# Optimization experiments

Hardware: AMD Instinct MI355X
Metric: run time of the kernel (lower is better)

The kernel has to match this reference:

```python
import jax, jax.numpy as jnp
import numpy as np

N_NODES = 50000


def _sage_conv(x, edge_index, W_l, W_r, b):
    """PyG SAGEConv (aggr='mean', root_weight=True):
    out[i] = mean_{j: (j->i) in E} x[j] @ W_l + x[i] @ W_r + b
    """
    src, dst = edge_index[0], edge_index[1]
    msgs = x[src]                                   # [E, d] gather
    agg = jax.ops.segment_sum(msgs, dst, num_segments=N_NODES)  # [N, d]
    deg = jax.ops.segment_sum(jnp.ones_like(dst, dtype=x.dtype), dst,
                              num_segments=N_NODES)
    agg = agg / jnp.maximum(deg, 1.0)[:, None]      # mean aggregation
    return agg @ W_l + x @ W_r + b


def setup_inputs() -> dict:
    key = jax.random.key(0)
    ks = jax.random.split(key, 8)
    d_in, d_hid, d_out = 128, 128, 64
    n_edges = 640000
    x = jax.random.normal(ks[0], (N_NODES, d_in), dtype=jnp.float32)
    edge_index = jax.random.randint(ks[1], (2, n_edges), 0, N_NODES, dtype=jnp.int32)
    s1 = 1.0 / np.sqrt(d_in)
    s2 = 1.0 / np.sqrt(d_hid)
    return {
        "x": x,
        "edge_index": edge_index,
        "W1_l": jax.random.uniform(ks[2], (d_in, d_hid), jnp.float32, -s1, s1),
        "W1_r": jax.random.uniform(ks[3], (d_in, d_hid), jnp.float32, -s1, s1),
        "b1": jnp.zeros((d_hid,), jnp.float32),
        "W2_l": jax.random.uniform(ks[4], (d_hid, d_out), jnp.float32, -s2, s2),
        "W2_r": jax.random.uniform(ks[5], (d_hid, d_out), jnp.float32, -s2, s2),
        "b2": jnp.zeros((d_out,), jnp.float32),
    }


def reference(x, edge_index, W1_l, W1_r, b1, W2_l, W2_r, b2):
    h = _sage_conv(x, edge_index, W1_l, W1_r, b1)
    h = jax.nn.relu(h)
    # Dropout(0.3) is identity in eval mode.
    return _sage_conv(h, edge_index, W2_l, W2_r, b2)
```

## Files before the change

kernel.cpp:

```cpp
#include <hip/hip_runtime.h>
#include <hip/hip_fp16.h>


typedef _Float16 half8 __attribute__((ext_vector_type(8)));
typedef float floatx4 __attribute__((ext_vector_type(4)));

#define NB 256
#define PA 320
#define HB 320

__global__ __launch_bounds__(256) void prep_hist_kernel(const float* __restrict__ x,
                                                        const float* __restrict__ W1l, const float* __restrict__ W1r,
                                                        const float* __restrict__ W2l, const float* __restrict__ W2r,
                                                        _Float16* __restrict__ Ah,
                                                        _Float16* __restrict__ Bp1, _Float16* __restrict__ Bp2,
                                                        const int* __restrict__ dst, int* __restrict__ ghist,
                                                        int N, int E, int nper) {
    __shared__ int lh[NB];
    int nconv = (N * 16 + 255) / 256;
    int b = blockIdx.x;
    int tid = threadIdx.x;
    if (b < nconv) {
        int i = b * 256 + tid;
        if (i < N * 16) {
            int row = i >> 4, c = i & 15;
            const float4* xp = (const float4*)x;
            float4 v0 = xp[(size_t)row * 32 + c * 2];
            float4 v1 = xp[(size_t)row * 32 + c * 2 + 1];
            __half2 h0 = __floats2half2_rn(v0.x, v0.y);
            __half2 h1 = __floats2half2_rn(v0.z, v0.w);
            __half2 h2 = __floats2half2_rn(v1.x, v1.y);
            __half2 h3 = __floats2half2_rn(v1.z, v1.w);
            uint4 o;
            o.x = *(const uint*)&h0; o.y = *(const uint*)&h1;
            o.z = *(const uint*)&h2; o.w = *(const uint*)&h3;
            *(uint4*)(Ah + (size_t)row * 256 + 128 + c * 8) = o;
        }
    } else if (b < nconv + 128) {
        int t = (b - nconv) * 256 + tid;
        int j = t & 7, lane = (t >> 3) & 63, nrep = (t >> 9) & 7, kt = t >> 12;
        int k = kt * 32 + ((lane >> 4) * 8) + j;
        int col = nrep * 16 + (lane & 15);
        float v = (k < 128) ? W1l[k * 128 + col] : W1r[(k - 128) * 128 + col];
        Bp1[t] = (_Float16)v;
    } else if (b < nconv + 192) {
        int t = (b - nconv - 128) * 256 + tid;
        int j = t & 7, lane = (t >> 3) & 63, nrep = (t >> 9) & 7, kt = t >> 12;
        int k = kt * 32 + ((lane >> 4) * 8) + j;
        int col = nrep * 16 + (lane & 15);
        float v = (col < 64) ? W2l[k * 64 + col] : W2r[k * 64 + (col - 64)];
        Bp2[t] = (_Float16)v;
    } else {
        int hb = b - nconv - 192;
        lh[tid] = 0;
        __syncthreads();
        int chunk = (E + HB - 1) / HB;
        int e0 = hb * chunk, e1 = min(e0 + chunk, E);
        for (int e = e0 + tid; e < e1; e += 256) atomicAdd(&lh[dst[e] / nper], 1);
        __syncthreads();
        int c = lh[tid];
        if (c) atomicAdd(&ghist[tid], c);
    }
}

__global__ __launch_bounds__(256) void partA_kernel(const int* __restrict__ src, const int* __restrict__ dst,
                                                    const int* __restrict__ ghist, int* __restrict__ bcur,
                                                    unsigned int* __restrict__ bek,
                                                    int E, int nper) {
    __shared__ int cnt[NB], base[NB], cur[NB];
    __shared__ int ws[4], wo[4];
    int tid = threadIdx.x;
    int v = ghist[tid];
    int lane = tid & 63, wid = tid >> 6;
    int s = v;
#pragma unroll
    for (int off = 1; off < 64; off <<= 1) { int t = __shfl_up(s, off); if (lane >= off) s += t; }
    if (lane == 63) ws[wid] = s;
    cnt[tid] = 0; cur[tid] = 0;
    __syncthreads();
    if (tid == 0) { int a = 0; for (int w = 0; w < 4; ++w) { wo[w] = a; a += ws[w]; } }
    __syncthreads();
    int excl = s + wo[wid] - v;
    int chunk = (E + PA - 1) / PA;
    int e0 = blockIdx.x * chunk;
    int e1 = min(e0 + chunk, E);
    for (int e = e0 + tid; e < e1; e += 256) {
        int d = dst[e];
        atomicAdd(&cnt[d / nper], 1);
    }
    __syncthreads();
    int c = cnt[tid];
    base[tid] = excl + ((c > 0) ? atomicAdd(&bcur[tid], c) : 0);
    __syncthreads();
    for (int e = e0 + tid; e < e1; e += 256) {
        int d = dst[e];
        int b = d / nper;
        int pos = base[b] + atomicAdd(&cur[b], 1);
        bek[pos] = ((unsigned int)src[e] << 8) | (unsigned int)(d - b * nper);
    }
}

__global__ __launch_bounds__(256) void partB2_kernel(const unsigned int* __restrict__ bek,
                                                     const int* __restrict__ ghist,
                                                     int* __restrict__ rp, float* __restrict__ inv,
                                                     int* __restrict__ csr, int N, int nper) {
    __shared__ int gh[NB], exg[NB];
    __shared__ int lcnt[256], excl[256], cur[256];
    __shared__ int ws[4], wo[4];
    int k = blockIdx.x;
    int lo = k * nper;
    int hi = min(lo + nper, N);
    int cntN = hi - lo;
    if (cntN <= 0) return;
    int tid = threadIdx.x;
    int lane = tid & 63, wid = tid >> 6;
    int v = ghist[tid];
    gh[tid] = v;
    int s = v;
#pragma unroll
    for (int off = 1; off < 64; off <<= 1) { int t = __shfl_up(s, off); if (lane >= off) s += t; }
    if (lane == 63) ws[wid] = s;
    lcnt[tid] = 0; cur[tid] = 0;
    __syncthreads();
    if (tid == 0) { int a = 0; for (int w = 0; w < 4; ++w) { wo[w] = a; a += ws[w]; } }
    __syncthreads();
    exg[tid] = s + wo[wid] - v;
    __syncthreads();
    int ebeg = exg[k], eend = ebeg + gh[k];
    for (int j = ebeg + tid; j < eend; j += 256)
        atomicAdd(&lcnt[bek[j] & 0xffu], 1);
    __syncthreads();
    int v2 = lcnt[tid];
    int s2 = v2;
#pragma unroll
    for (int off = 1; off < 64; off <<= 1) { int t = __shfl_up(s2, off); if (lane >= off) s2 += t; }
    if (lane == 63) ws[wid] = s2;
    __syncthreads();
    if (tid == 0) { int a = 0; for (int w = 0; w < 4; ++w) { wo[w] = a; a += ws[w]; } }
    __syncthreads();
    excl[tid] = s2 + wo[wid] - v2;
    __syncthreads();
    if (tid <= cntN) {
        int node = lo + tid;
        if (node <= N) rp[node] = ebeg + excl[tid];
        if (tid < cntN) inv[node] = 1.0f / fmaxf((float)lcnt[tid], 1.0f);
    }
    for (int j = ebeg + tid; j < eend; j += 256) {
        unsigned int u = bek[j];
        int loc = (int)(u & 0xffu);
        int pos = ebeg + excl[loc] + atomicAdd(&cur[loc], 1);
        csr[pos] = (int)(u >> 8);
    }
}

__global__ __launch_bounds__(256) void agg128h_kernel(const int* __restrict__ rp, const int* __restrict__ ci,
                                                      _Float16* __restrict__ Ah,
                                                      const float* __restrict__ inv, int N) {
    int node = (blockIdx.x * 256 + threadIdx.x) >> 6;
    int lane = threadIdx.x & 63;
    if (node >= N) return;
    int beg = rp[node], end = rp[node + 1];
    const uint* xu = (const uint*)Ah;
    float2 acc = make_float2(0.f, 0.f);
    for (int base = beg; base < end; base += 64) {
        int idx = base + lane;
        int sv = (idx < end) ? ci[idx] : 0;
        int cnt = min(64, end - base);
        int j = 0;
        for (; j + 8 <= cnt; j += 8) {
            uint u[8];
#pragma unroll
            for (int w = 0; w < 8; ++w) {
                int s = __shfl(sv, j + w);
                u[w] = xu[(size_t)s * 128 + 64 + lane];
            }
#pragma unroll
            for (int w = 0; w < 8; ++w) {
                float2 f = __half22float2(*(const __half2*)&u[w]);
                acc.x += f.x; acc.y += f.y;
            }
        }
        for (; j + 4 <= cnt; j += 4) {
            uint u[4];
#pragma unroll
            for (int w = 0; w < 4; ++w) {
                int s = __shfl(sv, j + w);
                u[w] = xu[(size_t)s * 128 + 64 + lane];
            }
#pragma unroll
            for (int w = 0; w < 4; ++w) {
                float2 f = __half22float2(*(const __half2*)&u[w]);
                acc.x += f.x; acc.y += f.y;
            }
        }
        for (; j < cnt; ++j) {
            int s = __shfl(sv, j);
            uint u = xu[(size_t)s * 128 + 64 + lane];
            float2 f = __half22float2(*(const __half2*)&u);
            acc.x += f.x; acc.y += f.y;
        }
    }
    float iv = inv[node];
    __half2 o = __floats2half2_rn(acc.x * iv, acc.y * iv);
    ((uint*)Ah)[(size_t)node * 128 + lane] = *(const uint*)&o;
}

__global__ __launch_bounds__(256) void agg64h_kernel(const int* __restrict__ rp, const int* __restrict__ ci,
                                                     const _Float16* __restrict__ hl,
                                                     const float* __restrict__ inv,
                                                     float* __restrict__ out, int N) {
    int node = (blockIdx.x * 256 + threadIdx.x) >> 5;
    int sl = threadIdx.x & 31;
    if (node >= N) return;
    int beg = rp[node], end = rp[node + 1];
    const uint* hu = (const uint*)hl;
    float2 acc = make_float2(0.f, 0.f);
    for (int base = beg; base < end; base += 32) {
        int idx = base + sl;
        int sv = (idx < end) ? ci[idx] : 0;
        int cnt = min(32, end - base);
        int j = 0;
        for (; j + 8 <= cnt; j += 8) {
            uint u[8];
#pragma unroll
            for (int w = 0; w < 8; ++w) {
                int s = __shfl(sv, j + w, 32);
                u[w] = hu[(size_t)s * 32 + sl];
            }
#pragma unroll
            for (int w = 0; w < 8; ++w) {
                float2 f = __half22float2(*(const __half2*)&u[w]);
                acc.x += f.x; acc.y += f.y;
            }
        }
        for (; j + 4 <= cnt; j += 4) {
            uint u[4];
#pragma unroll
            for (int w = 0; w < 4; ++w) {
                int s = __shfl(sv, j + w, 32);
                u[w] = hu[(size_t)s * 32 + sl];
            }
#pragma unroll
            for (int w = 0; w < 4; ++w) {
                float2 f = __half22float2(*(const __half2*)&u[w]);
                acc.x += f.x; acc.y += f.y;
            }
        }
        for (; j < cnt; ++j) {
            int s = __shfl(sv, j, 32);
            uint u = hu[(size_t)s * 32 + sl];
            float2 f = __half22float2(*(const __half2*)&u);
            acc.x += f.x; acc.y += f.y;
        }
    }
    float iv = inv[node];
    float2* op = (float2*)(out + (size_t)node * 64 + sl * 2);
    float2 cur = *op;
    cur.x += iv * acc.x;
    cur.y += iv * acc.y;
    *op = cur;
}

__global__ __launch_bounds__(256) void gemm1_mfma(const _Float16* __restrict__ Ah,
                                                  const _Float16* __restrict__ Bp,
                                                  const float* __restrict__ b1,
                                                  _Float16* __restrict__ hh, int N) {
    int wid = threadIdx.x >> 6, lane = threadIdx.x & 63;
    int r = lane & 15, q = lane >> 4;
    int rowbase = blockIdx.x * 128 + wid * 32;
    size_t ra = (size_t)min(rowbase + r, N - 1);
    size_t rb = (size_t)min(rowbase + 16 + r, N - 1);
    const half8* B8 = (const half8*)Bp;

    floatx4 acc[2][8];
#pragma unroll
    for (int m = 0; m < 2; ++m)
#pragma unroll
        for (int n = 0; n < 8; ++n) acc[m][n] = (floatx4){0.f, 0.f, 0.f, 0.f};

#pragma unroll
    for (int kt = 0; kt < 8; ++kt) {
        int k0 = kt * 32 + q * 8;
        half8 a0 = *(const half8*)(Ah + ra * 256 + k0);
        half8 a1 = *(const half8*)(Ah + rb * 256 + k0);
#pragma unroll
        for (int n = 0; n < 8; ++n) {
            half8 bf = B8[(kt * 8 + n) * 64 + lane];
            acc[0][n] = __builtin_amdgcn_mfma_f32_16x16x32_f16(a0, bf, acc[0][n], 0, 0, 0);
            acc[1][n] = __builtin_amdgcn_mfma_f32_16x16x32_f16(a1, bf, acc[1][n], 0, 0, 0);
        }
    }
    float bias[8];
#pragma unroll
    for (int n = 0; n < 8; ++n) bias[n] = b1[n * 16 + r];
#pragma unroll
    for (int m = 0; m < 2; ++m)
#pragma unroll
        for (int reg = 0; reg < 4; ++reg) {
            int row = rowbase + m * 16 + q * 4 + reg;
            if (row < N) {
                _Float16* p = hh + (size_t)row * 128 + r;
#pragma unroll
                for (int n = 0; n < 8; ++n)
                    p[n * 16] = (_Float16)fmaxf(acc[m][n][reg] + bias[n], 0.f);
            }
        }
}

__global__ __launch_bounds__(256) void gemm2_mfma(const _Float16* __restrict__ hh,
                                                  const _Float16* __restrict__ Bp,
                                                  const float* __restrict__ b2,
                                                  _Float16* __restrict__ hl,
                                                  float* __restrict__ outp, int N) {
    int wid = threadIdx.x >> 6, lane = threadIdx.x & 63;
    int r = lane & 15, q = lane >> 4;
    int rowbase = blockIdx.x * 128 + wid * 32;
    size_t ra = (size_t)min(rowbase + r, N - 1);
    size_t rb = (size_t)min(rowbase + 16 + r, N - 1);
    const half8* B8 = (const half8*)Bp;

    floatx4 acc[2][8];
#pragma unroll
    for (int m = 0; m < 2; ++m)
#pragma unroll
        for (int n = 0; n < 8; ++n) acc[m][n] = (floatx4){0.f, 0.f, 0.f, 0.f};

#pragma unroll
    for (int kt = 0; kt < 4; ++kt) {
        int k0 = kt * 32 + q * 8;
        half8 a0 = *(const half8*)(hh + ra * 128 + k0);
        half8 a1 = *(const half8*)(hh + rb * 128 + k0);
#pragma unroll
        for (int n = 0; n < 8; ++n) {
            half8 bf = B8[(kt * 8 + n) * 64 + lane];
            acc[0][n] = __builtin_amdgcn_mfma_f32_16x16x32_f16(a0, bf, acc[0][n], 0, 0, 0);
            acc[1][n] = __builtin_amdgcn_mfma_f32_16x16x32_f16(a1, bf, acc[1][n], 0, 0, 0);
        }
    }
    float bias[4];
#pragma unroll
    for (int n = 0; n < 4; ++n) bias[n] = b2[n * 16 + r];
#pragma unroll
    for (int m = 0; m < 2; ++m)
#pragma unroll
        for (int reg = 0; reg < 4; ++reg) {
            int row = rowbase + m * 16 + q * 4 + reg;
            if (row < N) {
                _Float16* ph = hl + (size_t)row * 64 + r;
                float* po = outp + (size_t)row * 64 + r;
#pragma unroll
                for (int n = 0; n < 4; ++n)
                    ph[n * 16] = (_Float16)acc[m][n][reg];
#pragma unroll
                for (int n = 0; n < 4; ++n)
                    po[n * 16] = acc[m][n + 4][reg] + bias[n];
            }
        }
}

extern "C" void kernel_launch(void* const* d_in, const int* in_sizes, int n_in,
                              void* d_out, int out_size, void* d_ws, size_t ws_size,
                              hipStream_t stream) {
    const float* x   = (const float*)d_in[0];
    const int*   ei  = (const int*)d_in[1];
    const float* W1l = (const float*)d_in[2];
    const float* W1r = (const float*)d_in[3];
    const float* b1  = (const float*)d_in[4];
    const float* W2l = (const float*)d_in[5];
    const float* W2r = (const float*)d_in[6];
    const float* b2  = (const float*)d_in[7];
    float* out = (float*)d_out;

    const int N = in_sizes[0] / 128;
    const int E = in_sizes[1] / 2;
    const int* srcv = ei;
    const int* dstv = ei + E;
    const int nper = (N + NB - 1) / NB;

    _Float16* Ah  = (_Float16*)d_ws;
    _Float16* hh  = Ah + (size_t)N * 256;
    _Float16* hl  = hh + (size_t)N * 128;
    _Float16* Bp1 = hl + (size_t)N * 64;
    _Float16* Bp2 = Bp1 + 32768;
    float* inv  = (float*)(Bp2 + 16384);
    int*   rp   = (int*)(inv + N);
    int*   csr  = rp + (N + 1);
    unsigned int* bek = (unsigned int*)(csr + E);
    int*   ghist = (int*)(bek + E);
    int*   bcur  = ghist + NB;

    hipMemsetAsync(ghist, 0, (size_t)(2 * NB) * sizeof(int), stream);

    int nconv = (N * 16 + 255) / 256;
    prep_hist_kernel<<<nconv + 192 + HB, 256, 0, stream>>>(x, W1l, W1r, W2l, W2r,
                                                           Ah, Bp1, Bp2, dstv, ghist, N, E, nper);

    partA_kernel<<<PA, 256, 0, stream>>>(srcv, dstv, ghist, bcur, bek, E, nper);
    partB2_kernel<<<NB, 256, 0, stream>>>(bek, ghist, rp, inv, csr, N, nper);

    agg128h_kernel<<<(N * 64 + 255) / 256, 256, 0, stream>>>(rp, csr, Ah, inv, N);
    int nb = (N + 127) / 128;
    gemm1_mfma<<<nb, 256, 0, stream>>>(Ah, Bp1, b1, hh, N);

    gemm2_mfma<<<nb, 256, 0, stream>>>(hh, Bp2, b2, hl, out, N);
    agg64h_kernel<<<(N * 32 + 255) / 256, 256, 0, stream>>>(rp, csr, hl, inv, out, N);
}
```

Before: 124.3 us.

## Fuse layer-1 and layer-2 GEMMs through shared-memory hidden tile

Merges the two MFMA GEMM kernels into one: the ReLU'd layer-1 hidden tile of each wave is written to LDS instead of global memory, then read back as the A operand for the layer-2 GEMM. This removes the global write and read of the N×128 fp16 hidden tensor and one kernel launch. In exchange it uses about 34 KB of LDS per block, which may reduce occupancy, and it makes the fused kernel longer and heavier on registers. Each wave only reads its own LDS region, so no block barrier is needed.

```diff
diff --git a/kernel.cpp b/kernel.cpp
--- a/kernel.cpp
+++ b/kernel.cpp
@@ -261,16 +261,21 @@
     *op = cur;
 }
 
-__global__ __launch_bounds__(256) void gemm1_mfma(const _Float16* __restrict__ Ah,
-                                                  const _Float16* __restrict__ Bp,
-                                                  const float* __restrict__ b1,
-                                                  _Float16* __restrict__ hh, int N) {
+__global__ __launch_bounds__(256) void gemm12_mfma(const _Float16* __restrict__ Ah,
+                                                   const _Float16* __restrict__ Bp1,
+                                                   const _Float16* __restrict__ Bp2,
+                                                   const float* __restrict__ b1,
+                                                   const float* __restrict__ b2,
+                                                   _Float16* __restrict__ hl,
+                                                   float* __restrict__ outp, int N) {
+    __shared__ _Float16 hlds[4][32][136];
     int wid = threadIdx.x >> 6, lane = threadIdx.x & 63;
     int r = lane & 15, q = lane >> 4;
     int rowbase = blockIdx.x * 128 + wid * 32;
     size_t ra = (size_t)min(rowbase + r, N - 1);
     size_t rb = (size_t)min(rowbase + 16 + r, N - 1);
-    const half8* B8 = (const half8*)Bp;
+    const half8* B8a = (const half8*)Bp1;
+    const half8* B8b = (const half8*)Bp2;
 
     floatx4 acc[2][8];
 #pragma unroll
@@ -285,54 +290,39 @@
         half8 a1 = *(const half8*)(Ah + rb * 256 + k0);
 #pragma unroll
         for (int n = 0; n < 8; ++n) {
-            half8 bf = B8[(kt * 8 + n) * 64 + lane];
+            half8 bf = B8a[(kt * 8 + n) * 64 + lane];
             acc[0][n] = __builtin_amdgcn_mfma_f32_16x16x32_f16(a0, bf, acc[0][n], 0, 0, 0);
             acc[1][n] = __builtin_amdgcn_mfma_f32_16x16x32_f16(a1, bf, acc[1][n], 0, 0, 0);
         }
     }
-    float bias[8];
-#pragma unroll
-    for (int n = 0; n < 8; ++n) bias[n] = b1[n * 16 + r];
-#pragma unroll
-    for (int m = 0; m < 2; ++m)
-#pragma unroll
-        for (int reg = 0; reg < 4; ++reg) {
-            int row = rowbase + m * 16 + q * 4 + reg;
-            if (row < N) {
-                _Float16* p = hh + (size_t)row * 128 + r;
+    {
+        float bias[8];
+#pragma unroll
+        for (int n = 0; n < 8; ++n) bias[n] = b1[n * 16 + r];
+#pragma unroll
+        for (int m = 0; m < 2; ++m)
+#pragma unroll
+            for (int reg = 0; reg < 4; ++reg) {
+                int rl = m * 16 + q * 4 + reg;
+                _Float16* p = &hlds[wid][rl][r];
 #pragma unroll
                 for (int n = 0; n < 8; ++n)
                     p[n * 16] = (_Float16)fmaxf(acc[m][n][reg] + bias[n], 0.f);
             }
-        }
-}
-
-__global__ __launch_bounds__(256) void gemm2_mfma(const _Float16* __restrict__ hh,
-                                                  const _Float16* __restrict__ Bp,
-                                                  const float* __restrict__ b2,
-                                                  _Float16* __restrict__ hl,
-                                                  float* __restrict__ outp, int N) {
-    int wid = threadIdx.x >> 6, lane = threadIdx.x & 63;
-    int r = lane & 15, q = lane >> 4;
-    int rowbase = blockIdx.x * 128 + wid * 32;
-    size_t ra = (size_t)min(rowbase + r, N - 1);
-    size_t rb = (size_t)min(rowbase + 16 + r, N - 1);
-    const half8* B8 = (const half8*)Bp;
-
-    floatx4 acc[2][8];
+    }
+
 #pragma unroll
     for (int m = 0; m < 2; ++m)
 #pragma unroll
         for (int n = 0; n < 8; ++n) acc[m][n] = (floatx4){0.f, 0.f, 0.f, 0.f};
-
 #pragma unroll
     for (int kt = 0; kt < 4; ++kt) {
         int k0 = kt * 32 + q * 8;
-        half8 a0 = *(const half8*)(hh + ra * 128 + k0);
-        half8 a1 = *(const half8*)(hh + rb * 128 + k0);
+        half8 a0 = *(const half8*)&hlds[wid][r][k0];
+        half8 a1 = *(const half8*)&hlds[wid][16 + r][k0];
 #pragma unroll
         for (int n = 0; n < 8; ++n) {
-            half8 bf = B8[(kt * 8 + n) * 64 + lane];
+            half8 bf = B8b[(kt * 8 + n) * 64 + lane];
             acc[0][n] = __builtin_amdgcn_mfma_f32_16x16x32_f16(a0, bf, acc[0][n], 0, 0, 0);
             acc[1][n] = __builtin_amdgcn_mfma_f32_16x16x32_f16(a1, bf, acc[1][n], 0, 0, 0);
         }
@@ -378,8 +368,7 @@
     const int nper = (N + NB - 1) / NB;
 
     _Float16* Ah  = (_Float16*)d_ws;
-    _Float16* hh  = Ah + (size_t)N * 256;
-    _Float16* hl  = hh + (size_t)N * 128;
+    _Float16* hl  = Ah + (size_t)N * 256;
     _Float16* Bp1 = hl + (size_t)N * 64;
     _Float16* Bp2 = Bp1 + 32768;
     float* inv  = (float*)(Bp2 + 16384);
@@ -399,9 +388,9 @@
     partB2_kernel<<<NB, 256, 0, stream>>>(bek, ghist, rp, inv, csr, N, nper);
 
     agg128h_kernel<<<(N * 64 + 255) / 256, 256, 0, stream>>>(rp, csr, Ah, inv, N);
+
     int nb = (N + 127) / 128;
-    gemm1_mfma<<<nb, 256, 0, stream>>>(Ah, Bp1, b1, hh, N);
-
-    gemm2_mfma<<<nb, 256, 0, stream>>>(hh, Bp2, b2, hl, out, N);
+    gemm12_mfma<<<nb, 256, 0, stream>>>(Ah, Bp1, Bp2, b1, b2, hl, out, N);
+
     agg64h_kernel<<<(N * 32 + 255) / 256, 256, 0, stream>>>(rp, csr, hl, inv, out, N);
 }
```

After: 131.7 us. 6.0% more time.
